# Optimization experiments

Hardware: AMD Instinct MI355X
Metric: run time of the kernel (lower is better)

Reference implementation:

```python
import jax, jax.numpy as jnp
import numpy as np

PAD_ID, SOS_ID, EOS_ID = 0, 1, 2


def setup_inputs() -> dict:
    key = jax.random.key(0)
    ks = jax.random.split(key, 8)
    V, E, H, B = 16000, 256, 512, 8
    s = 0.05  # weight scale to keep softmax well-conditioned
    return {
        "hidden": jax.random.normal(ks[0], (1, B, H), dtype=jnp.float32),
        "embedding": jax.random.normal(ks[1], (V, E), dtype=jnp.float32) * s,
        "w_ih": jax.random.normal(ks[2], (3 * H, E), dtype=jnp.float32) * s,
        "w_hh": jax.random.normal(ks[3], (3 * H, H), dtype=jnp.float32) * s,
        "b_ih": jax.random.normal(ks[4], (3 * H,), dtype=jnp.float32) * s,
        "b_hh": jax.random.normal(ks[5], (3 * H,), dtype=jnp.float32) * s,
        "w_out": jax.random.normal(ks[6], (V, H), dtype=jnp.float32) * s,
        "b_out": jax.random.normal(ks[7], (V,), dtype=jnp.float32) * s,
        "lenseq": 12,
        "k": 5,
    }


def reference(hidden, embedding, w_ih, w_hh, b_ih, b_hh, w_out, b_out, lenseq, k):
    V, E = embedding.shape
    _, B, H = hidden.shape
    dt = hidden.dtype
    pad_onehot = jax.nn.one_hot(PAD_ID, V, dtype=dt)

    def gru_cell(x_emb, h):  # x_emb: (k,B,E), h: (k,B,H); torch nn.GRU gate order r,z,n
        gi = x_emb @ w_ih.T + b_ih
        gh = h @ w_hh.T + b_hh
        i_r, i_z, i_n = jnp.split(gi, 3, axis=-1)
        h_r, h_z, h_n = jnp.split(gh, 3, axis=-1)
        r = jax.nn.sigmoid(i_r + h_r)
        z = jax.nn.sigmoid(i_z + h_z)
        n = jnp.tanh(i_n + r * h_n)
        return (1.0 - z) * n + z * h

    def step(carry, i):
        x, h, prob, res, _ = carry
        done = (x == EOS_ID) | (x == PAD_ID)            # (k,B)
        emb = embedding[x]                               # (k,B,E)
        h_new = gru_cell(emb, h)                         # (k,B,H)
        probs = jax.nn.softmax(h_new @ w_out.T + b_out, axis=-1)  # (k,B,V)
        pred = jnp.where(done[..., None], pad_onehot, probs)
        h = jnp.where(done[..., None], h, h_new)
        res = res.at[:, i].set(pred)                     # store raw pred (pre prob-scaling), as torch.cat copies
        scores = pred * prob[..., None]                  # (k,B,V); prob stays all-ones, faithful to source
        flat = scores.transpose(1, 0, 2).reshape(B, k * V)  # beam-major flatten per batch elem
        _, idx = jax.lax.top_k(flat, k)                  # (B,k)
        beam = (idx // V).T                              # (k,B)
        tok = (idx % V).T                                # (k,B)
        res = jnp.take_along_axis(res, beam[:, None, :, None], axis=0)
        prob = jnp.take_along_axis(prob, beam, axis=0)
        h = jnp.take_along_axis(h, beam[..., None], axis=0)
        return (tok, h, prob, res, pred), None

    x0 = jnp.full((k, B), SOS_ID, dtype=jnp.int32)
    h0 = jnp.broadcast_to(hidden[0], (k, B, H))
    prob0 = jnp.ones((k, B), dtype=dt)
    res0 = jnp.zeros((k, lenseq, B, V), dtype=dt)
    pred0 = jnp.zeros((k, B, V), dtype=dt)

    (x, h, prob, res, pred), _ = jax.lax.scan(step, (x0, h0, prob0, res0, pred0), jnp.arange(lenseq))

    # final top-1 selection per batch element over (k*V) flat scores
    scores = pred * prob[..., None]
    flat = scores.transpose(1, 0, 2).reshape(B, k * V)
    best_beam = jnp.argmax(flat, axis=-1) // V           # (B,)
    out = jnp.take_along_axis(res, best_beam[None, None, :, None], axis=0)[0]  # (lenseq,B,V)
    return out
```

## Files before the change

kernel.cpp:

```cpp
#include <hip/hip_runtime.h>

#define V 16000
#define E 256
#define H 512
#define HP 516
#define BB 8
#define T 12
#define NB 256
#define TPB 1024
#define CPB 63
#define AGENT __HIP_MEMORY_SCOPE_AGENT


constexpr int W_FL   = CPB * 512;
constexpr int SH_OFF = W_FL;
constexpr int SP_OFF = SH_OFF + BB * HP;
constexpr int RS_OFF = SP_OFF + 64 * 48;
constexpr int RV_OFF = RS_OFF + 128;
constexpr int RI_OFF = RV_OFF + 128;
constexpr int SS_OFF = RI_OFF + 128;
constexpr int XN_OFF = SS_OFF + 8;
constexpr int X_OFF  = XN_OFF + 8;
constexpr int SMEM_FL = X_OFF + 8;
constexpr size_t SMEM_BYTES = (size_t)SMEM_FL * 4;

__device__ __forceinline__ float dot4(float4 a, float4 b) {
    return a.x * b.x + a.y * b.y + a.z * b.z + a.w * b.w;
}

__global__ __launch_bounds__(256) void kinit(const float* __restrict__ hidden,
                                             float* __restrict__ hA,
                                             int* __restrict__ leaf,
                                             int* __restrict__ epoch) {
    int idx = blockIdx.x * 256 + threadIdx.x;
    if (idx < BB * H) hA[idx] = hidden[idx];
    if (idx < 64 * 16) leaf[idx] = 0;
    if (idx == 0) epoch[0] = 0;
}

__device__ __forceinline__ void gridbar(int* __restrict__ leaf,
                                        int* __restrict__ epoch, int ep) {
    __syncthreads();
    if (threadIdx.x == 0) {
        int g = blockIdx.x >> 2;
        __hip_atomic_fetch_add(&leaf[g * 16], 1, __ATOMIC_RELEASE, AGENT);
    }
    if (blockIdx.x == 0) {
        if (threadIdx.x < 64) {
            while (__hip_atomic_load(&leaf[threadIdx.x * 16],
                                     __ATOMIC_RELAXED, AGENT) < 4 * ep)
                __builtin_amdgcn_s_sleep(1);
        }
        __syncthreads();
        if (threadIdx.x == 0)
            __hip_atomic_store(epoch, ep, __ATOMIC_RELAXED, AGENT);
    } else {
        if (threadIdx.x == 0) {
            while (__hip_atomic_load(epoch, __ATOMIC_RELAXED, AGENT) < ep)
                __builtin_amdgcn_s_sleep(1);
        }
    }
    __builtin_amdgcn_fence(__ATOMIC_ACQUIRE, "workgroup");
    __syncthreads();
}

__global__ __launch_bounds__(TPB, 4) void kmain(
    const float* __restrict__ emb_tab,
    const float* __restrict__ w_ih,
    const float* __restrict__ w_hh,
    const float* __restrict__ b_ih,
    const float* __restrict__ b_hh,
    const float* __restrict__ w_out,
    const float* __restrict__ b_out,
    float* __restrict__ hA,
    float* __restrict__ hB,
    float* __restrict__ psum,
    float* __restrict__ pval,
    int* __restrict__ pidx,
    int* __restrict__ leaf,
    int* __restrict__ epoch,
    float* __restrict__ out)
{
    extern __shared__ float smem[];
    float* w_lds  = smem;
    float* s_h    = smem + SH_OFF;
    float* s_part = smem + SP_OFF;
    float* s_rsum = smem + RS_OFF;
    float* s_rval = smem + RV_OFF;
    int*   s_ridx = (int*)(smem + RI_OFF);
    float* s_S    = smem + SS_OFF;
    int*   s_Xn   = (int*)(smem + XN_OFF);
    int*   s_X    = (int*)(smem + X_OFF);

    const int blk = blockIdx.x, tid = threadIdx.x;

    for (int i = tid; i < CPB * 128; i += TPB) {
        int col = i >> 7;
        int q4  = (i & 127) << 2;
        int vv  = blk * CPB + col;
        if (vv < V) {
            float4 w4 = *(const float4*)(w_out + (size_t)vv * H + q4);
            *(float4*)(w_lds + col * 512 + (q4 ^ ((col & 7) << 2))) = w4;
        }
    }
    if (tid < BB) s_X[tid] = 1;
    __syncthreads();

    const int lane = tid & 63;
    const int wv   = tid >> 6;
    const int r    = lane & 7;
    const int kh   = (lane >> 3) & 1;
    const int colw = (lane >> 4) & 3;
    const int col  = wv * 4 + colw;
    const int v    = blk * CPB + col;
    const bool ok  = (col < CPB) && (v < V);
    const int ca   = ok ? col : 0;
    const int swz  = (ca & 7) << 2;
    float e = 0.f;

    for (int t = 0; t < T; t++) {
        const float* h_cur = (t & 1) ? hB : hA;
        float*       h_nxt = (t & 1) ? hA : hB;
        const int par = t & 1;

        if (blk < 64) {
            int hr = tid >> 7, k4 = (tid & 127) << 2;
            const unsigned long long* p =
                (const unsigned long long*)(h_cur + hr * H + k4);
            union { unsigned long long u; float f[2]; } c0, c1;
            c0.u = __hip_atomic_load(p,     __ATOMIC_RELAXED, AGENT);
            c1.u = __hip_atomic_load(p + 1, __ATOMIC_RELAXED, AGENT);
            s_h[hr * HP + k4]     = c0.f[0]; s_h[hr * HP + k4 + 1] = c0.f[1];
            s_h[hr * HP + k4 + 2] = c1.f[0]; s_h[hr * HP + k4 + 3] = c1.f[1];
        }
        __syncthreads();
        if (blk < 64 && tid < 512) {
            const int jl = tid >> 6;
            const int ar = (tid >> 3) & 7;
            const int kq = tid & 7;
            const int j  = blk * 8 + jl;
            const int pair = jl * 8 + ar;
            float gir = 0.f, giz = 0.f, gin = 0.f, ghr = 0.f, ghz = 0.f, ghn = 0.f;
            {
                const float* erow = emb_tab + (size_t)s_X[ar] * E;
                const float* w0 = w_ih + (size_t)j * E;
                const float* w1 = w0 + (size_t)H * E;
                const float* w2 = w1 + (size_t)H * E;
                const int k0 = kq * (E / 8);
                for (int k = 0; k < E / 8; k += 4) {
                    float4 ev = *(const float4*)(erow + k0 + k);
                    gir += dot4(*(const float4*)(w0 + k0 + k), ev);
                    giz += dot4(*(const float4*)(w1 + k0 + k), ev);
                    gin += dot4(*(const float4*)(w2 + k0 + k), ev);
                }
            }
            {
                const float* hrow = s_h + ar * HP;
                const float* w0 = w_hh + (size_t)j * H;
                const float* w1 = w0 + (size_t)H * H;
                const float* w2 = w1 + (size_t)H * H;
                const int k0 = kq * (H / 8);
                for (int k = 0; k < H / 8; k += 4) {
                    float4 hv = *(const float4*)(hrow + k0 + k);
                    ghr += dot4(*(const float4*)(w0 + k0 + k), hv);
                    ghz += dot4(*(const float4*)(w1 + k0 + k), hv);
                    ghn += dot4(*(const float4*)(w2 + k0 + k), hv);
                }
            }
            float* sp = s_part + pair * 48;
            sp[0 * 8 + kq] = gir; sp[1 * 8 + kq] = giz; sp[2 * 8 + kq] = gin;
            sp[3 * 8 + kq] = ghr; sp[4 * 8 + kq] = ghz; sp[5 * 8 + kq] = ghn;
        }
        __syncthreads();
        if (blk < 64 && tid < 512 && (tid & 7) == 0) {
            const int pair = (tid >> 6) * 8 + ((tid >> 3) & 7);
            const int jl = pair >> 3, ar = pair & 7;
            const int j  = blk * 8 + jl;
            const float* sp2 = s_part + pair * 48;
            float G[6];
#pragma unroll
            for (int gg = 0; gg < 6; gg++) {
                float s = 0.f;
#pragma unroll
                for (int q = 0; q < 8; q++) s += sp2[gg * 8 + q];
                G[gg] = s;
            }
            float ir  = G[0] + b_ih[j],         hr_ = G[3] + b_hh[j];
            float iz  = G[1] + b_ih[H + j],     hz  = G[4] + b_hh[H + j];
            float inn = G[2] + b_ih[2 * H + j], hn  = G[5] + b_hh[2 * H + j];
            float rg = 1.f / (1.f + __expf(-(ir + hr_)));
            float zg = 1.f / (1.f + __expf(-(iz + hz)));
            float ng = tanhf(inn + rg * hn);
            float ho = s_h[ar * HP + j];
            int xr = s_X[ar];
            bool dn = (xr == 0) || (xr == 2);
            float hv = dn ? ho : ((1.f - zg) * ng + zg * ho);
            __hip_atomic_store(&h_nxt[ar * H + j], hv, __ATOMIC_RELAXED, AGENT);
        }
        gridbar(leaf, epoch, 2 * t + 1);

        {
            int hr = tid >> 7, k4 = (tid & 127) << 2;
            const unsigned long long* p =
                (const unsigned long long*)(h_nxt + hr * H + k4);
            union { unsigned long long u; float f[2]; } c0, c1;
            c0.u = __hip_atomic_load(p,     __ATOMIC_RELAXED, AGENT);
            c1.u = __hip_atomic_load(p + 1, __ATOMIC_RELAXED, AGENT);
            s_h[hr * HP + k4]     = c0.f[0]; s_h[hr * HP + k4 + 1] = c0.f[1];
            s_h[hr * HP + k4 + 2] = c1.f[0]; s_h[hr * HP + k4 + 3] = c1.f[1];
        }
        __syncthreads();
        {
            const float* wb = w_lds + ca * 512;
            const float* hb = s_h + r * HP + kh * 256;
            float acc = 0.f;
            for (int q = 0; q < 256; q += 4) {
                float4 w4 = *(const float4*)(wb + ((kh * 256 + q) ^ swz));
                float4 h4 = *(const float4*)(hb + q);
                acc += dot4(w4, h4);
            }
            float other = __shfl_xor(acc, 8, 64);
            float lo = kh ? other : acc;
            float hi = kh ? acc : other;
            e = __expf(lo + hi + (ok ? b_out[v] : 0.f));

            float s  = (ok && kh == 0) ? e : 0.f;
            float bv = (ok && kh == 0) ? e : -1.f;
            int   bi = (ok && kh == 0) ? v : 0x7fffffff;
#pragma unroll
            for (int m = 8; m <= 32; m <<= 1) {
                s += __shfl_xor(s, m, 64);
                float ov = __shfl_xor(bv, m, 64);
                int   oi = __shfl_xor(bi, m, 64);
                if (ov > bv || (ov == bv && oi < bi)) { bv = ov; bi = oi; }
            }
            if ((lane >> 3) == 0) {
                s_rsum[wv * 8 + r] = s;
                s_rval[wv * 8 + r] = bv;
                s_ridx[wv * 8 + r] = bi;
            }
        }
        __syncthreads();
        if (tid < 64) {
            float s  = s_rsum[tid] + s_rsum[tid + 64];
            float av = s_rval[tid], bv2 = s_rval[tid + 64];
            int   ai = s_ridx[tid], bi2 = s_ridx[tid + 64];
            float bv = av; int bi = ai;
            if (bv2 > bv || (bv2 == bv && bi2 < bi)) { bv = bv2; bi = bi2; }
#pragma unroll
            for (int m = 8; m <= 32; m <<= 1) {
                s += __shfl_xor(s, m, 64);
                float ov = __shfl_xor(bv, m, 64);
                int   oi = __shfl_xor(bi, m, 64);
                if (ov > bv || (ov == bv && oi < bi)) { bv = ov; bi = oi; }
            }
            if (tid < 8) {
                int o = (par * 8 + tid) * NB + blk;
                __hip_atomic_store(&psum[o], s,  __ATOMIC_RELAXED, AGENT);
                __hip_atomic_store(&pval[o], bv, __ATOMIC_RELAXED, AGENT);
                __hip_atomic_store(&pidx[o], bi, __ATOMIC_RELAXED, AGENT);
            }
        }
        gridbar(leaf, epoch, 2 * t + 2);

        if (wv < 8) {
            const int base = (par * 8 + wv) * NB;
            float s = 0.f, bv = -1.f; int bi = 0x7fffffff;
#pragma unroll
            for (int c = 0; c < 4; c++) {
                int o = base + lane + 64 * c;
                s += __hip_atomic_load(&psum[o], __ATOMIC_RELAXED, AGENT);
                float ov = __hip_atomic_load(&pval[o], __ATOMIC_RELAXED, AGENT);
                int   oi = __hip_atomic_load(&pidx[o], __ATOMIC_RELAXED, AGENT);
                if (ov > bv || (ov == bv && oi < bi)) { bv = ov; bi = oi; }
            }
            for (int m = 1; m < 64; m <<= 1) {
                s += __shfl_xor(s, m, 64);
                float ov = __shfl_xor(bv, m, 64);
                int   oi = __shfl_xor(bi, m, 64);
                if (ov > bv || (ov == bv && oi < bi)) { bv = ov; bi = oi; }
            }
            if (lane == 0) { s_S[wv] = s; s_Xn[wv] = bi; }
        }
        __syncthreads();
        {
            float* out_t = out + (size_t)t * BB * V;
            int xr = s_X[r];
            bool dn = (xr == 0) || (xr == 2);
            float inv = 1.f / s_S[r];
            if (ok && kh == 0) {
                float val = dn ? ((v == 0) ? 1.f : 0.f) : e * inv;
                __builtin_nontemporal_store(val, out_t + r * V + v);
            }
        }
        __syncthreads();
        if (tid < 8) {
            int xo = s_X[tid];
            s_X[tid] = ((xo == 0) || (xo == 2)) ? 0 : s_Xn[tid];
        }
        __syncthreads();
    }
}

extern "C" void kernel_launch(void* const* d_in, const int* in_sizes, int n_in,
                              void* d_out, int out_size, void* d_ws, size_t ws_size,
                              hipStream_t stream) {
    (void)in_sizes; (void)n_in; (void)out_size; (void)ws_size;
    const float* hidden    = (const float*)d_in[0];
    const float* embedding = (const float*)d_in[1];
    const float* w_ih      = (const float*)d_in[2];
    const float* w_hh      = (const float*)d_in[3];
    const float* b_ih      = (const float*)d_in[4];
    const float* b_hh      = (const float*)d_in[5];
    const float* w_out     = (const float*)d_in[6];
    const float* b_out     = (const float*)d_in[7];
    float* out = (float*)d_out;

    float* ws    = (float*)d_ws;
    float* hA    = ws;
    float* hB    = hA + BB * H;
    float* psum  = hB + BB * H;
    float* pval  = psum + 2 * 8 * NB;
    int*   pidx  = (int*)(pval + 2 * 8 * NB);
    int*   leaf  = pidx + 2 * 8 * NB;
    int*   epoch = leaf + 64 * 16;

    static bool attr_set = false;
    hipFuncSetAttribute((const void*)kmain,
        hipFuncAttributeMaxDynamicSharedMemorySize,
        (int)SMEM_BYTES);
    (void)attr_set;

    kinit<<<16, 256, 0, stream>>>(hidden, hA, leaf, epoch);
    kmain<<<NB, TPB, SMEM_BYTES, stream>>>(embedding, w_ih, w_hh, b_ih, b_hh,
                                           w_out, b_out, hA, hB, psum, pval,
                                           pidx, leaf, epoch, out);
}
```

Before: 581.7 us.

## Restructure output projection to keep h in registers across eight columns

Result: slower. 693.4 us (+19.2%).

```diff
diff --git a/kernel.cpp b/kernel.cpp
--- a/kernel.cpp
+++ b/kernel.cpp
@@ -100,7 +100,8 @@
         int vv  = blk * CPB + col;
         if (vv < V) {
             float4 w4 = *(const float4*)(w_out + (size_t)vv * H + q4);
-            *(float4*)(w_lds + col * 512 + (q4 ^ ((col & 7) << 2))) = w4;
+            int sw = q4 ^ ((col & 7) << 2) ^ (((q4 >> 5) & 7) << 2);
+            *(float4*)(w_lds + col * 512 + sw) = w4;
         }
     }
     if (tid < BB) s_X[tid] = 1;
@@ -108,20 +109,19 @@
 
     const int lane = tid & 63;
     const int wv   = tid >> 6;
-    const int r    = lane & 7;
-    const int kh   = (lane >> 3) & 1;
-    const int colw = (lane >> 4) & 3;
-    const int col  = wv * 4 + colw;
-    const int v    = blk * CPB + col;
-    const bool ok  = (col < CPB) && (v < V);
-    const int ca   = ok ? col : 0;
-    const int swz  = (ca & 7) << 2;
-    float e = 0.f;
+    const int rh   = lane & 3;
+    const int kq   = (lane >> 2) & 15;
+    const int rowhalf = wv & 1;
+    const int cs   = wv >> 1;
+    const int r    = rowhalf * 4 + rh;
+    const int xw   = (cs ^ (kq & 7)) << 2;
+    const int hswz = (kq & 7) << 2;
 
     for (int t = 0; t < T; t++) {
         const float* h_cur = (t & 1) ? hB : hA;
         float*       h_nxt = (t & 1) ? hA : hB;
         const int par = t & 1;
+        float e_arr[8];
 
         if (blk < 64) {
             int hr = tid >> 7, k4 = (tid & 127) << 2;
@@ -130,14 +130,14 @@
             union { unsigned long long u; float f[2]; } c0, c1;
             c0.u = __hip_atomic_load(p,     __ATOMIC_RELAXED, AGENT);
             c1.u = __hip_atomic_load(p + 1, __ATOMIC_RELAXED, AGENT);
-            s_h[hr * HP + k4]     = c0.f[0]; s_h[hr * HP + k4 + 1] = c0.f[1];
-            s_h[hr * HP + k4 + 2] = c1.f[0]; s_h[hr * HP + k4 + 3] = c1.f[1];
+            *(float4*)(s_h + hr * HP + k4) =
+                make_float4(c0.f[0], c0.f[1], c1.f[0], c1.f[1]);
         }
         __syncthreads();
         if (blk < 64 && tid < 512) {
             const int jl = tid >> 6;
             const int ar = (tid >> 3) & 7;
-            const int kq = tid & 7;
+            const int kq8 = tid & 7;
             const int j  = blk * 8 + jl;
             const int pair = jl * 8 + ar;
             float gir = 0.f, giz = 0.f, gin = 0.f, ghr = 0.f, ghz = 0.f, ghn = 0.f;
@@ -146,7 +146,7 @@
                 const float* w0 = w_ih + (size_t)j * E;
                 const float* w1 = w0 + (size_t)H * E;
                 const float* w2 = w1 + (size_t)H * E;
-                const int k0 = kq * (E / 8);
+                const int k0 = kq8 * (E / 8);
                 for (int k = 0; k < E / 8; k += 4) {
                     float4 ev = *(const float4*)(erow + k0 + k);
                     gir += dot4(*(const float4*)(w0 + k0 + k), ev);
@@ -159,7 +159,7 @@
                 const float* w0 = w_hh + (size_t)j * H;
                 const float* w1 = w0 + (size_t)H * H;
                 const float* w2 = w1 + (size_t)H * H;
-                const int k0 = kq * (H / 8);
+                const int k0 = kq8 * (H / 8);
                 for (int k = 0; k < H / 8; k += 4) {
                     float4 hv = *(const float4*)(hrow + k0 + k);
                     ghr += dot4(*(const float4*)(w0 + k0 + k), hv);
@@ -168,8 +168,8 @@
                 }
             }
             float* sp = s_part + pair * 48;
-            sp[0 * 8 + kq] = gir; sp[1 * 8 + kq] = giz; sp[2 * 8 + kq] = gin;
-            sp[3 * 8 + kq] = ghr; sp[4 * 8 + kq] = ghz; sp[5 * 8 + kq] = ghn;
+            sp[0 * 8 + kq8] = gir; sp[1 * 8 + kq8] = giz; sp[2 * 8 + kq8] = gin;
+            sp[3 * 8 + kq8] = ghr; sp[4 * 8 + kq8] = ghz; sp[5 * 8 + kq8] = ghn;
         }
         __syncthreads();
         if (blk < 64 && tid < 512 && (tid & 7) == 0) {
@@ -206,38 +206,51 @@
             union { unsigned long long u; float f[2]; } c0, c1;
             c0.u = __hip_atomic_load(p,     __ATOMIC_RELAXED, AGENT);
             c1.u = __hip_atomic_load(p + 1, __ATOMIC_RELAXED, AGENT);
-            s_h[hr * HP + k4]     = c0.f[0]; s_h[hr * HP + k4 + 1] = c0.f[1];
-            s_h[hr * HP + k4 + 2] = c1.f[0]; s_h[hr * HP + k4 + 3] = c1.f[1];
+            int sw = k4 ^ (((k4 >> 5) & 7) << 2);
+            *(float4*)(s_h + hr * HP + sw) =
+                make_float4(c0.f[0], c0.f[1], c1.f[0], c1.f[1]);
         }
         __syncthreads();
         {
-            const float* wb = w_lds + ca * 512;
-            const float* hb = s_h + r * HP + kh * 256;
-            float acc = 0.f;
-            for (int q = 0; q < 256; q += 4) {
-                float4 w4 = *(const float4*)(wb + ((kh * 256 + q) ^ swz));
-                float4 h4 = *(const float4*)(hb + q);
-                acc += dot4(w4, h4);
-            }
-            float other = __shfl_xor(acc, 8, 64);
-            float lo = kh ? other : acc;
-            float hi = kh ? acc : other;
-            e = __expf(lo + hi + (ok ? b_out[v] : 0.f));
-
-            float s  = (ok && kh == 0) ? e : 0.f;
-            float bv = (ok && kh == 0) ? e : -1.f;
-            int   bi = (ok && kh == 0) ? v : 0x7fffffff;
-#pragma unroll
-            for (int m = 8; m <= 32; m <<= 1) {
-                s += __shfl_xor(s, m, 64);
-                float ov = __shfl_xor(bv, m, 64);
-                int   oi = __shfl_xor(bi, m, 64);
-                if (ov > bv || (ov == bv && oi < bi)) { bv = ov; bi = oi; }
-            }
-            if ((lane >> 3) == 0) {
-                s_rsum[wv * 8 + r] = s;
+            float4 hreg[8];
+            const float* hb = s_h + r * HP + kq * 32;
+#pragma unroll
+            for (int i = 0; i < 8; i++)
+                hreg[i] = *(const float4*)(hb + ((4 * i) ^ hswz));
+
+            float s_acc = 0.f, bv = -1.f; int bi = 0x7fffffff;
+#pragma unroll
+            for (int p = 0; p < 8; p++) {
+                const int col = p * 8 + cs;
+                const int vv  = blk * CPB + col;
+                const bool okp = (col < CPB) && (vv < V);
+                const int cc = okp ? col : 0;
+                const float* wb = w_lds + cc * 512 + kq * 32;
+                float acc = 0.f;
+#pragma unroll
+                for (int i = 0; i < 8; i++) {
+                    float4 w4 = *(const float4*)(wb + ((4 * i) ^ xw));
+                    acc += dot4(w4, hreg[i]);
+                }
+                acc += __shfl_xor(acc, 4, 64);
+                acc += __shfl_xor(acc, 8, 64);
+                acc += __shfl_xor(acc, 16, 64);
+                acc += __shfl_xor(acc, 32, 64);
+                float ee = 0.f;
+                if (okp) ee = __expf(acc + b_out[vv]);
+                e_arr[p] = ee;
+                s_acc += ee;
+                if (ee > bv) { bv = ee; bi = vv; }
+            }
+            if (kq == 0) {
+                s_rsum[wv * 8 + r] = s_acc;
                 s_rval[wv * 8 + r] = bv;
                 s_ridx[wv * 8 + r] = bi;
+            } else if (kq == 1) {
+                int ro = (1 - rowhalf) * 4 + rh;
+                s_rsum[wv * 8 + ro] = 0.f;
+                s_rval[wv * 8 + ro] = -1.f;
+                s_ridx[wv * 8 + ro] = 0x7fffffff;
             }
         }
         __syncthreads();
@@ -288,9 +301,17 @@
             int xr = s_X[r];
             bool dn = (xr == 0) || (xr == 2);
             float inv = 1.f / s_S[r];
-            if (ok && kh == 0) {
-                float val = dn ? ((v == 0) ? 1.f : 0.f) : e * inv;
-                __builtin_nontemporal_store(val, out_t + r * V + v);
+            if (lane < 4) {
+#pragma unroll
+                for (int p = 0; p < 8; p++) {
+                    int col = p * 8 + cs;
+                    int vv  = blk * CPB + col;
+                    if (col < CPB && vv < V) {
+                        float val = dn ? ((vv == 0) ? 1.f : 0.f)
+                                       : e_arr[p] * inv;
+                        __builtin_nontemporal_store(val, out_t + r * V + vv);
+                    }
+                }
             }
         }
         __syncthreads();
@@ -325,11 +346,9 @@
     int*   leaf  = pidx + 2 * 8 * NB;
     int*   epoch = leaf + 64 * 16;
 
-    static bool attr_set = false;
     hipFuncSetAttribute((const void*)kmain,
         hipFuncAttributeMaxDynamicSharedMemorySize,
         (int)SMEM_BYTES);
-    (void)attr_set;
 
     kinit<<<16, 256, 0, stream>>>(hidden, hA, leaf, epoch);
     kmain<<<NB, TPB, SMEM_BYTES, stream>>>(embedding, w_ih, w_hh, b_ih, b_hh,
```
